# Kernel tuning notes

Measured on AMD Instinct MI355X. Metric: run time of the kernel, lower is better.

## Reference

```python
import jax, jax.numpy as jnp
import numpy as np

B, S, D, H = 4, 2048, 512, 8
DK = D // H


def setup_inputs() -> dict:
    key = jax.random.key(0)
    ks = jax.random.split(key, 8)
    std = 1.0 / np.sqrt(D)
    return {
        "query": jax.random.normal(ks[0], (B, S, D), jnp.float32),
        "key": jax.random.normal(ks[1], (B, S, D), jnp.float32),
        "value": jax.random.normal(ks[2], (B, S, D), jnp.float32),
        "Wq": jax.random.normal(ks[3], (D, D), jnp.float32) * std,
        "Wk": jax.random.normal(ks[4], (D, D), jnp.float32) * std,
        "Wv": jax.random.normal(ks[5], (D, D), jnp.float32) * std,
        "Wo": jax.random.normal(ks[6], (D, D), jnp.float32) * std,
        "bo": jnp.zeros((D,), jnp.float32),
    }


def reference(query, key, value, Wq, Wk, Wv, Wo, bo):
    # nn.Linear stores weight [out, in]; y = x @ W.T
    def split_heads(x):  # [B,S,D] -> [B,H,S,DK]
        return x.reshape(B, S, H, DK).transpose(0, 2, 1, 3)

    Q = split_heads(query @ Wq.T)
    K = split_heads(key @ Wk.T)
    V = split_heads(value @ Wv.T)
    scale = jnp.sqrt(jnp.asarray(DK, Q.dtype))
    scores = jnp.einsum("bhqd,bhkd->bhqk", Q, K) / scale  # [B,H,S,S]
    attn = jax.nn.softmax(scores, axis=-1)  # dropout=0 / eval mode
    ctx = jnp.einsum("bhqk,bhkd->bhqd", attn, V)
    ctx = ctx.transpose(0, 2, 1, 3).reshape(B, S, D)
    return ctx @ Wo.T + bo
```

## Files before the change

### kernel.cpp

```cpp
#include <hip/hip_runtime.h>
#include <hip/hip_bf16.h>
#include <stdint.h>

#define DEV __device__ __forceinline__

typedef __attribute__((ext_vector_type(8))) __bf16 bf16x8;
typedef __attribute__((ext_vector_type(4))) float f32x4;
typedef __attribute__((ext_vector_type(16))) float f32x16;
typedef __attribute__((ext_vector_type(4))) short short4v;
typedef __attribute__((ext_vector_type(8))) short short8v;
typedef __attribute__((ext_vector_type(4))) unsigned int uint4v;
typedef __attribute__((ext_vector_type(2))) unsigned int uint2v;

constexpr int B_ = 4, S_ = 2048, D_ = 512, H_ = 8, DK_ = 64;
constexpr int M_ = B_ * S_;
constexpr int K_ = D_;

DEV unsigned short f2bf(float f) {
  unsigned int u = __builtin_bit_cast(unsigned int, f);
  unsigned int r = (u + 0x7fffu + ((u >> 16) & 1u)) >> 16;
  return (unsigned short)r;
}

DEV void gld16(const void* g, void* l) {
  __builtin_amdgcn_global_load_lds(
      (const __attribute__((address_space(1))) unsigned int*)g,
      (__attribute__((address_space(3))) unsigned int*)l, 16, 0, 0);
}

DEV f32x4 mfma16(bf16x8 a, bf16x8 b, f32x4 c) {
  return __builtin_amdgcn_mfma_f32_16x16x32_bf16(a, b, c, 0, 0, 0);
}
DEV f32x16 mfma32(bf16x8 a, bf16x8 b, f32x16 c) {
  return __builtin_amdgcn_mfma_f32_32x32x16_bf16(a, b, c, 0, 0, 0);
}

DEV short4v tr16(const void* p) {
  short4v d;
  asm volatile("ds_read_b64_tr_b16 %0, %1"
               : "=v"(d)
               : "v"((const __attribute__((address_space(3))) char*)p));
  return d;
}

DEV unsigned pkbf(float a, float b) {
  unsigned r;
  asm("v_cvt_pk_bf16_f32 %0, %1, %2" : "=v"(r) : "v"(a), "v"(b));
  return r;
}

DEV void pl32swap(unsigned& a, unsigned& b) {
  asm volatile("v_permlane32_swap_b32 %0, %1" : "+v"(a), "+v"(b));
}

__global__ __launch_bounds__(256) void convert_w(
    const float* __restrict__ w0, const float* __restrict__ w1,
    const float* __restrict__ w2, const float* __restrict__ w3,
    unsigned short* __restrict__ o0, unsigned short* __restrict__ o1,
    unsigned short* __restrict__ o2, unsigned short* __restrict__ o3)
{
  int u = blockIdx.x * 256 + threadIdx.x;
  int t = u >> 16, off = (u & 65535) * 4;
  const float* src = (t == 0) ? w0 : (t == 1) ? w1 : (t == 2) ? w2 : w3;
  unsigned short* dst = (t == 0) ? o0 : (t == 1) ? o1 : (t == 2) ? o2 : o3;
  float4 f = *(const float4*)(src + off);
  short4v o;
  o.x = (short)f2bf(f.x); o.y = (short)f2bf(f.y);
  o.z = (short)f2bf(f.z); o.w = (short)f2bf(f.w);
  *(short4v*)(dst + off) = o;
}

__global__ __launch_bounds__(256, 3) void gemm_qkv(
    const float* __restrict__ A0, const float* __restrict__ A1,
    const float* __restrict__ A2,
    const unsigned short* __restrict__ W0, const unsigned short* __restrict__ W1,
    const unsigned short* __restrict__ W2,
    unsigned short* __restrict__ O0, unsigned short* __restrict__ O1,
    unsigned short* __restrict__ O2)
{
  constexpr int BM = 128, BN = 128, BK = 64, NKT = K_ / BK;
  __shared__ unsigned short As[BM * BK];
  __shared__ unsigned short Bs[BN * BK];
  const int tid = threadIdx.x, lane = tid & 63, wave = tid >> 6;
  const int z = blockIdx.z;
  const float* A = (z == 0) ? A0 : (z == 1 ? A1 : A2);
  const unsigned short* W = (z == 0) ? W0 : (z == 1 ? W1 : W2);
  unsigned short* outH = (z == 0) ? O0 : (z == 1 ? O1 : O2);
  const int bn0 = blockIdx.x * BN, bm0 = blockIdx.y * BM;
  const int wr = (wave >> 1) * 64, wc = (wave & 1) * 64;
  const int frow = lane & 15, fk16 = (lane >> 4) * 16;

  const int srow = tid >> 1, scol = (tid & 1) * 32;
  const float* asrc = A + (size_t)(bm0 + srow) * K_ + scol;
  const int abase = srow * 128 + scol * 2, asw = (srow & 7) << 4;

  const char* srcB[4];
  int dstB[4];
#pragma unroll
  for (int i = 0; i < 4; ++i) {
    int o = (wave * 4 + i) * 1024;
    int ol = o + lane * 16;
    int row = ol >> 7, off = (ol ^ ((row & 7) << 4)) & 127;
    srcB[i] = (const char*)W + (size_t)(bn0 + row) * (K_ * 2) + off;
    dstB[i] = o;
  }

  f32x4 acc[4][4];
#pragma unroll
  for (int i = 0; i < 4; ++i)
#pragma unroll
    for (int j = 0; j < 4; ++j)
#pragma unroll
      for (int r = 0; r < 4; ++r) acc[i][j][r] = 0.f;

  float4 xv[8];
#pragma unroll
  for (int j = 0; j < 8; ++j) xv[j] = *(const float4*)(asrc + j * 4);

  for (int kt = 0; kt < NKT; ++kt) {
    __syncthreads();
    {
      unsigned dw[16];
#pragma unroll
      for (int j = 0; j < 8; ++j) {
        dw[2 * j]     = pkbf(xv[j].x, xv[j].y);
        dw[2 * j + 1] = pkbf(xv[j].z, xv[j].w);
      }
#pragma unroll
      for (int c = 0; c < 4; ++c) {
        uint4v q = {dw[4 * c], dw[4 * c + 1], dw[4 * c + 2], dw[4 * c + 3]};
        *(uint4v*)((char*)As + ((abase + c * 16) ^ asw)) = q;
      }
    }
#pragma unroll
    for (int i = 0; i < 4; ++i) gld16(srcB[i] + kt * 128, (char*)Bs + dstB[i]);
    __syncthreads();
    if (kt + 1 < NKT) {
#pragma unroll
      for (int j = 0; j < 8; ++j)
        xv[j] = *(const float4*)(asrc + (kt + 1) * 64 + j * 4);
    }
#pragma unroll
    for (int kc = 0; kc < 2; ++kc) {
      bf16x8 a[4], b[4];
#pragma unroll
      for (int i = 0; i < 4; ++i) {
        int row = wr + i * 16 + frow;
        a[i] = *(const bf16x8*)((const char*)As +
                ((row * 128 + kc * 64 + fk16) ^ ((row & 7) << 4)));
      }
#pragma unroll
      for (int j = 0; j < 4; ++j) {
        int row = wc + j * 16 + frow;
        b[j] = *(const bf16x8*)((const char*)Bs +
                ((row * 128 + kc * 64 + fk16) ^ ((row & 7) << 4)));
      }
      __builtin_amdgcn_s_setprio(1);
#pragma unroll
      for (int i = 0; i < 4; ++i)
#pragma unroll
        for (int j = 0; j < 4; ++j)
          acc[i][j] = mfma16(a[i], b[j], acc[i][j]);
      __builtin_amdgcn_s_setprio(0);
    }
  }

  const int r0 = (lane >> 4) * 4, cn = lane & 15;
#pragma unroll
  for (int i = 0; i < 4; ++i)
#pragma unroll
    for (int j = 0; j < 4; ++j)
#pragma unroll
      for (int r = 0; r < 4; ++r) {
        int gm = bm0 + wr + i * 16 + r0 + r;
        int gn = bn0 + wc + j * 16 + cn;
        outH[(size_t)gm * D_ + gn] = f2bf(acc[i][j][r]);
      }
}

__global__ __launch_bounds__(256, 4) void gemm_out(
    const unsigned short* __restrict__ A, const unsigned short* __restrict__ W,
    float* __restrict__ outF, const float* __restrict__ bias)
{
  constexpr int BM = 64, BN = 128, BK = 64, NKT = K_ / BK, AFR = 2;
  __shared__ unsigned short As[BM * BK];
  __shared__ unsigned short Bs[BN * BK];
  const int tid = threadIdx.x, lane = tid & 63, wave = tid >> 6;
  const int bn0 = blockIdx.x * BN, bm0 = blockIdx.y * BM;
  const int wr = (wave >> 1) * 32, wc = (wave & 1) * 64;
  const int frow = lane & 15, fk16 = (lane >> 4) * 16;

  const char* srcA[AFR];
  int dstA[AFR];
#pragma unroll
  for (int i = 0; i < AFR; ++i) {
    int o = (wave * AFR + i) * 1024;
    int ol = o + lane * 16;
    int row = ol >> 7, off = (ol ^ ((row & 7) << 4)) & 127;
    srcA[i] = (const char*)A + (size_t)(bm0 + row) * (K_ * 2) + off;
    dstA[i] = o;
  }
  const char* srcB[4];
  int dstB[4];
#pragma unroll
  for (int i = 0; i < 4; ++i) {
    int o = (wave * 4 + i) * 1024;
    int ol = o + lane * 16;
    int row = ol >> 7, off = (ol ^ ((row & 7) << 4)) & 127;
    srcB[i] = (const char*)W + (size_t)(bn0 + row) * (K_ * 2) + off;
    dstB[i] = o;
  }

  f32x4 acc[AFR][4];
#pragma unroll
  for (int i = 0; i < AFR; ++i)
#pragma unroll
    for (int j = 0; j < 4; ++j)
#pragma unroll
      for (int r = 0; r < 4; ++r) acc[i][j][r] = 0.f;

  for (int kt = 0; kt < NKT; ++kt) {
    __syncthreads();
#pragma unroll
    for (int i = 0; i < AFR; ++i) gld16(srcA[i] + kt * 128, (char*)As + dstA[i]);
#pragma unroll
    for (int i = 0; i < 4; ++i)   gld16(srcB[i] + kt * 128, (char*)Bs + dstB[i]);
    __syncthreads();
#pragma unroll
    for (int kc = 0; kc < 2; ++kc) {
      bf16x8 a[AFR], b[4];
#pragma unroll
      for (int i = 0; i < AFR; ++i) {
        int row = wr + i * 16 + frow;
        a[i] = *(const bf16x8*)((const char*)As +
                ((row * 128 + kc * 64 + fk16) ^ ((row & 7) << 4)));
      }
#pragma unroll
      for (int j = 0; j < 4; ++j) {
        int row = wc + j * 16 + frow;
        b[j] = *(const bf16x8*)((const char*)Bs +
                ((row * 128 + kc * 64 + fk16) ^ ((row & 7) << 4)));
      }
      __builtin_amdgcn_s_setprio(1);
#pragma unroll
      for (int i = 0; i < AFR; ++i)
#pragma unroll
        for (int j = 0; j < 4; ++j)
          acc[i][j] = mfma16(a[i], b[j], acc[i][j]);
      __builtin_amdgcn_s_setprio(0);
    }
  }

  const int r0 = (lane >> 4) * 4, cn = lane & 15;
  float bv[4];
#pragma unroll
  for (int j = 0; j < 4; ++j) bv[j] = bias[bn0 + wc + j * 16 + cn];
#pragma unroll
  for (int i = 0; i < AFR; ++i)
#pragma unroll
    for (int j = 0; j < 4; ++j)
#pragma unroll
      for (int r = 0; r < 4; ++r) {
        int gm = bm0 + wr + i * 16 + r0 + r;
        int gn = bn0 + wc + j * 16 + cn;
        outF[(size_t)gm * D_ + gn] = acc[i][j][r] + bv[j];
      }
}

__global__ __launch_bounds__(256, 2) void attn(
    const unsigned short* __restrict__ Qm, const unsigned short* __restrict__ Km,
    const unsigned short* __restrict__ Vm, unsigned short* __restrict__ Ctx)
{
  constexpr int QB = 128, KVB = 64, NT = S_ / KVB;
  __shared__ unsigned short Qs[QB * DK_];
  __shared__ unsigned short Kd[2][KVB * DK_];
  __shared__ unsigned short Vd[2][KVB * DK_];
  const int tid = threadIdx.x, lane = tid & 63, wave = tid >> 6;
  const int hi = lane >> 5, l31 = lane & 31, g1 = (lane >> 4) & 1;
  const int bh = blockIdx.y, q0 = blockIdx.x * QB;
  const int bq = bh >> 3, hh = bh & 7;
  const char* Qg = (const char*)(Qm + ((size_t)bq * S_ + q0) * D_ + hh * DK_);
  const char* Kg = (const char*)(Km + (size_t)bq * S_ * D_ + hh * DK_);
  const char* Vg = (const char*)(Vm + (size_t)bq * S_ * D_ + hh * DK_);

  auto stageSwz = [&](const char* gbase, unsigned short* lds, int o) {
    int ol = o + lane * 16;
    int row = ol >> 7, off = (ol ^ ((row & 7) << 4)) & 127;
    gld16(gbase + (size_t)row * 1024 + off, (char*)lds + o);
  };
  auto stageVt = [&](const char* gbase, unsigned short* lds, int o) {
    int ol = o + lane * 16;
    int E0 = ol >> 1;
    int st = E0 >> 6, rr = (E0 >> 4) & 3, c0 = E0 & 15;
    int kk = (st >> 2) * 4 + rr, dd = (st & 3) * 16 + c0;
    gld16(gbase + (size_t)kk * 1024 + dd * 2, (char*)lds + o);
  };

#pragma unroll
  for (int i = 0; i < 4; ++i) stageSwz(Qg, Qs, (wave * 4 + i) * 1024);
#pragma unroll
  for (int i = 0; i < 2; ++i) stageSwz(Kg, Kd[0], (wave * 2 + i) * 1024);
#pragma unroll
  for (int i = 0; i < 2; ++i) stageVt(Vg, Vd[0], (wave * 2 + i) * 1024);
  __syncthreads();

  bf16x8 qf[4];
  {
    int row = wave * 32 + l31;
    int rb = row * 128, sw = (row & 7) << 4;
#pragma unroll
    for (int c = 0; c < 4; ++c)
      qf[c] = *(const bf16x8*)((const char*)Qs + ((rb + c * 32 + hi * 16) ^ sw));
  }

  f32x16 oacc[2];
#pragma unroll
  for (int dt = 0; dt < 2; ++dt)
#pragma unroll
    for (int r = 0; r < 16; ++r) oacc[dt][r] = 0.f;
  float m2 = -1e30f, lsum = 0.f;
  constexpr float SCL2 = 0.125f * 1.44269504089f;

  short4v va[4][2][2];
  bf16x8 pfrag[4];
#pragma unroll
  for (int c = 0; c < 4; ++c) {
#pragma unroll
    for (int dt = 0; dt < 2; ++dt) {
      va[c][dt][0] = short4v{0, 0, 0, 0};
      va[c][dt][1] = short4v{0, 0, 0, 0};
    }
    uint4v zz = {0u, 0u, 0u, 0u};
    pfrag[c] = __builtin_bit_cast(bf16x8, zz);
  }

  int cur = 0;
  for (int t = 0; t < NT; ++t) {
    if (t + 1 < NT) {
      const char* Kg1 = Kg + (size_t)(t + 1) * KVB * 1024;
      const char* Vg1 = Vg + (size_t)(t + 1) * KVB * 1024;
#pragma unroll
      for (int i = 0; i < 2; ++i) stageSwz(Kg1, Kd[cur ^ 1], (wave * 2 + i) * 1024);
#pragma unroll
      for (int i = 0; i < 2; ++i) stageVt(Vg1, Vd[cur ^ 1], (wave * 2 + i) * 1024);
    }

    f32x16 sacc[2];
#pragma unroll
    for (int k2 = 0; k2 < 2; ++k2)
#pragma unroll
      for (int r = 0; r < 16; ++r) sacc[k2][r] = 0.f;
    __builtin_amdgcn_s_setprio(1);
#pragma unroll
    for (int c = 0; c < 4; ++c) {
#pragma unroll
      for (int k2 = 0; k2 < 2; ++k2) {
        int row = k2 * 32 + l31;
        bf16x8 kf = *(const bf16x8*)((const char*)Kd[cur] +
                     ((row * 128 + c * 32 + hi * 16) ^ ((row & 7) << 4)));
        sacc[k2] = mfma32(kf, qf[c], sacc[k2]);
      }
    }
#pragma unroll
    for (int c = 0; c < 4; ++c)
#pragma unroll
      for (int dt = 0; dt < 2; ++dt) {
        short8v vv = __builtin_shufflevector(va[c][dt][0], va[c][dt][1],
                                             0, 1, 2, 3, 4, 5, 6, 7);
        oacc[dt] = mfma32(__builtin_bit_cast(bf16x8, vv), pfrag[c], oacc[dt]);
      }
    __builtin_amdgcn_s_setprio(0);

    float mloc = sacc[0][0];
#pragma unroll
    for (int k2 = 0; k2 < 2; ++k2)
#pragma unroll
      for (int r = 0; r < 16; ++r) mloc = fmaxf(mloc, sacc[k2][r]);
    mloc = fmaxf(mloc, __shfl_xor(mloc, 32));
    float m2n = fmaxf(m2, mloc * SCL2);
    float alpha = __builtin_amdgcn_exp2f(m2 - m2n);
    m2 = m2n;
    float psum = 0.f;
#pragma unroll
    for (int k2 = 0; k2 < 2; ++k2)
#pragma unroll
      for (int r = 0; r < 16; ++r) {
        float p = __builtin_amdgcn_exp2f(fmaf(sacc[k2][r], SCL2, -m2n));
        sacc[k2][r] = p;
        psum += p;
      }
    psum += __shfl_xor(psum, 32);
    lsum = lsum * alpha + psum;

#pragma unroll
    for (int dt = 0; dt < 2; ++dt)
#pragma unroll
      for (int r = 0; r < 16; ++r) oacc[dt][r] *= alpha;

#pragma unroll
    for (int c = 0; c < 4; ++c)
#pragma unroll
      for (int dt = 0; dt < 2; ++dt) {
        int st = 16 * c + 8 * hi + 2 * dt + g1;
        const char* ad = (const char*)Vd[cur] + st * 128 + (lane & 15) * 8;
        va[c][dt][0] = tr16(ad);
        va[c][dt][1] = tr16(ad + 512);
      }
#pragma unroll
    for (int c = 0; c < 4; ++c) {
      const f32x16& P = sacc[c >> 1];
      const int b = (c & 1) * 8;
      unsigned d0 = pkbf(P[b + 0], P[b + 1]);
      unsigned d1 = pkbf(P[b + 2], P[b + 3]);
      unsigned d2 = pkbf(P[b + 4], P[b + 5]);
      unsigned d3 = pkbf(P[b + 6], P[b + 7]);
      pl32swap(d0, d2);
      pl32swap(d1, d3);
      uint4v pi = {d0, d1, d2, d3};
      pfrag[c] = __builtin_bit_cast(bf16x8, pi);
    }

    __syncthreads();
    cur ^= 1;
  }

  __builtin_amdgcn_s_setprio(1);
#pragma unroll
  for (int c = 0; c < 4; ++c)
#pragma unroll
    for (int dt = 0; dt < 2; ++dt) {
      short8v vv = __builtin_shufflevector(va[c][dt][0], va[c][dt][1],
                                           0, 1, 2, 3, 4, 5, 6, 7);
      oacc[dt] = mfma32(__builtin_bit_cast(bf16x8, vv), pfrag[c], oacc[dt]);
    }
  __builtin_amdgcn_s_setprio(0);

  const float inv = 1.f / lsum;
  unsigned short* crow =
      Ctx + ((size_t)bq * S_ + q0 + wave * 32 + l31) * D_ + hh * DK_;
#pragma unroll
  for (int dt = 0; dt < 2; ++dt)
#pragma unroll
    for (int g = 0; g < 4; ++g) {
      uint2v pk;
      pk.x = pkbf(oacc[dt][4 * g + 0] * inv, oacc[dt][4 * g + 1] * inv);
      pk.y = pkbf(oacc[dt][4 * g + 2] * inv, oacc[dt][4 * g + 3] * inv);
      *(uint2v*)(crow + dt * 32 + 8 * g + 4 * hi) = pk;
    }
}

extern "C" void kernel_launch(void* const* d_in, const int* in_sizes, int n_in,
                              void* d_out, int out_size, void* d_ws, size_t ws_size,
                              hipStream_t stream) {
  const float* q  = (const float*)d_in[0];
  const float* k  = (const float*)d_in[1];
  const float* v  = (const float*)d_in[2];
  const float* wq = (const float*)d_in[3];
  const float* wk = (const float*)d_in[4];
  const float* wv = (const float*)d_in[5];
  const float* wo = (const float*)d_in[6];
  const float* bo = (const float*)d_in[7];
  float* out = (float*)d_out;

  constexpr size_t NX = (size_t)M_ * D_;
  constexpr size_t NW = (size_t)D_ * D_;
  char* ws = (char*)d_ws;
  unsigned short* Wqb = (unsigned short*)ws; ws += NW * 2;
  unsigned short* Wkb = (unsigned short*)ws; ws += NW * 2;
  unsigned short* Wvb = (unsigned short*)ws; ws += NW * 2;
  unsigned short* Wob = (unsigned short*)ws; ws += NW * 2;
  unsigned short* Qbf = (unsigned short*)ws; ws += NX * 2;
  unsigned short* Kbf = (unsigned short*)ws; ws += NX * 2;
  unsigned short* Vbf = (unsigned short*)ws; ws += NX * 2;
  unsigned short* Cx  = (unsigned short*)ws; ws += NX * 2;

  convert_w<<<1024, 256, 0, stream>>>(wq, wk, wv, wo, Wqb, Wkb, Wvb, Wob);
  gemm_qkv<<<dim3(4, 64, 3), 256, 0, stream>>>(
      q, k, v, Wqb, Wkb, Wvb, Qbf, Kbf, Vbf);
  attn<<<dim3(S_ / 128, B_ * H_), 256, 0, stream>>>(Qbf, Kbf, Vbf, Cx);
  gemm_out<<<dim3(4, 128), 256, 0, stream>>>(Cx, Wob, out, bo);
}
```

Before: 201.0 us.

## Add lazy softmax rescaling and precompute LDS addresses in attention loop

Precomputes the global source and LDS destination addresses for K/V staging outside the loop, uses immediate offsets for transposed LDS reads, and unrolls the loop by two so the double-buffer indices are compile-time constants. It also adds a lazy online-softmax rescale: the running max and the accumulator rescale are updated only when some lane's new max exceeds the old one by more than 8 in log2 units. The row-sum uses four partial sums and the max uses a tree reduction to shorten dependency chains. The cost is extra code size, plus exponentials that can reach up to 2^8 before a rescale.

```diff
diff --git a/kernel.cpp b/kernel.cpp
--- a/kernel.cpp
+++ b/kernel.cpp
@@ -35,11 +35,12 @@
   return __builtin_amdgcn_mfma_f32_32x32x16_bf16(a, b, c, 0, 0, 0);
 }
 
-DEV short4v tr16(const void* p) {
+template <int OFF>
+DEV short4v tr16o(const void* p) {
   short4v d;
-  asm volatile("ds_read_b64_tr_b16 %0, %1"
+  asm volatile("ds_read_b64_tr_b16 %0, %1 offset:%2"
                : "=v"(d)
-               : "v"((const __attribute__((address_space(3))) char*)p));
+               : "v"((const __attribute__((address_space(3))) char*)p), "i"(OFF));
   return d;
 }
 
@@ -283,25 +284,38 @@
   const char* Kg = (const char*)(Km + (size_t)bq * S_ * D_ + hh * DK_);
   const char* Vg = (const char*)(Vm + (size_t)bq * S_ * D_ + hh * DK_);
 
-  auto stageSwz = [&](const char* gbase, unsigned short* lds, int o) {
+  const char* srcK[2];
+  const char* srcV[2];
+  int dstKV[2];
+#pragma unroll
+  for (int i = 0; i < 2; ++i) {
+    int o = (wave * 2 + i) * 1024;
+    int ol = o + lane * 16;
+    {
+      int row = ol >> 7, off = (ol ^ ((row & 7) << 4)) & 127;
+      srcK[i] = Kg + (size_t)row * 1024 + off;
+    }
+    {
+      int E0 = ol >> 1;
+      int st = E0 >> 6, rr = (E0 >> 4) & 3, c0 = E0 & 15;
+      int kk = (st >> 2) * 4 + rr, dd = (st & 3) * 16 + c0;
+      srcV[i] = Vg + (size_t)kk * 1024 + dd * 2;
+    }
+    dstKV[i] = o;
+  }
+
+#pragma unroll
+  for (int i = 0; i < 4; ++i) {
+    int o = (wave * 4 + i) * 1024;
     int ol = o + lane * 16;
     int row = ol >> 7, off = (ol ^ ((row & 7) << 4)) & 127;
-    gld16(gbase + (size_t)row * 1024 + off, (char*)lds + o);
-  };
-  auto stageVt = [&](const char* gbase, unsigned short* lds, int o) {
-    int ol = o + lane * 16;
-    int E0 = ol >> 1;
-    int st = E0 >> 6, rr = (E0 >> 4) & 3, c0 = E0 & 15;
-    int kk = (st >> 2) * 4 + rr, dd = (st & 3) * 16 + c0;
-    gld16(gbase + (size_t)kk * 1024 + dd * 2, (char*)lds + o);
-  };
-
-#pragma unroll
-  for (int i = 0; i < 4; ++i) stageSwz(Qg, Qs, (wave * 4 + i) * 1024);
-#pragma unroll
-  for (int i = 0; i < 2; ++i) stageSwz(Kg, Kd[0], (wave * 2 + i) * 1024);
-#pragma unroll
-  for (int i = 0; i < 2; ++i) stageVt(Vg, Vd[0], (wave * 2 + i) * 1024);
+    gld16(Qg + (size_t)row * 1024 + off, (char*)Qs + o);
+  }
+#pragma unroll
+  for (int i = 0; i < 2; ++i) {
+    gld16(srcK[i], (char*)Kd[0] + dstKV[i]);
+    gld16(srcV[i], (char*)Vd[0] + dstKV[i]);
+  }
   __syncthreads();
 
   bf16x8 qf[4];
@@ -313,6 +327,13 @@
       qf[c] = *(const bf16x8*)((const char*)Qs + ((rb + c * 32 + hi * 16) ^ sw));
   }
 
+  int bofs[4];
+  {
+    const int swk = (l31 & 7) << 4;
+#pragma unroll
+    for (int c = 0; c < 4; ++c) bofs[c] = (c * 32 + hi * 16) ^ swk;
+  }
+
   f32x16 oacc[2];
 #pragma unroll
   for (int dt = 0; dt < 2; ++dt)
@@ -334,15 +355,15 @@
     pfrag[c] = __builtin_bit_cast(bf16x8, zz);
   }
 
-  int cur = 0;
-  for (int t = 0; t < NT; ++t) {
-    if (t + 1 < NT) {
-      const char* Kg1 = Kg + (size_t)(t + 1) * KVB * 1024;
-      const char* Vg1 = Vg + (size_t)(t + 1) * KVB * 1024;
-#pragma unroll
-      for (int i = 0; i < 2; ++i) stageSwz(Kg1, Kd[cur ^ 1], (wave * 2 + i) * 1024);
-#pragma unroll
-      for (int i = 0; i < 2; ++i) stageVt(Vg1, Vd[cur ^ 1], (wave * 2 + i) * 1024);
+  auto tile = [&](const unsigned short* Kbuf, const unsigned short* Vbuf,
+                  unsigned short* KbufN, unsigned short* VbufN,
+                  int tnext, bool doStage) {
+    if (doStage) {
+#pragma unroll
+      for (int i = 0; i < 2; ++i) {
+        gld16(srcK[i] + (size_t)tnext * 65536, (char*)KbufN + dstKV[i]);
+        gld16(srcV[i] + (size_t)tnext * 65536, (char*)VbufN + dstKV[i]);
+      }
     }
 
     f32x16 sacc[2];
@@ -350,16 +371,14 @@
     for (int k2 = 0; k2 < 2; ++k2)
 #pragma unroll
       for (int r = 0; r < 16; ++r) sacc[k2][r] = 0.f;
+    const char* kb = (const char*)Kbuf + l31 * 128;
     __builtin_amdgcn_s_setprio(1);
 #pragma unroll
     for (int c = 0; c < 4; ++c) {
-#pragma unroll
-      for (int k2 = 0; k2 < 2; ++k2) {
-        int row = k2 * 32 + l31;
-        bf16x8 kf = *(const bf16x8*)((const char*)Kd[cur] +
-                     ((row * 128 + c * 32 + hi * 16) ^ ((row & 7) << 4)));
-        sacc[k2] = mfma32(kf, qf[c], sacc[k2]);
-      }
+      bf16x8 kf0 = *(const bf16x8*)(kb + bofs[c]);
+      bf16x8 kf1 = *(const bf16x8*)(kb + bofs[c] + 4096);
+      sacc[0] = mfma32(kf0, qf[c], sacc[0]);
+      sacc[1] = mfma32(kf1, qf[c], sacc[1]);
     }
 #pragma unroll
     for (int c = 0; c < 4; ++c)
@@ -371,41 +390,45 @@
       }
     __builtin_amdgcn_s_setprio(0);
 
-    float mloc = sacc[0][0];
+    float mx[16];
+#pragma unroll
+    for (int r = 0; r < 16; ++r) mx[r] = fmaxf(sacc[0][r], sacc[1][r]);
+#pragma unroll
+    for (int st = 8; st >= 1; st >>= 1)
+#pragma unroll
+      for (int r = 0; r < st; ++r) mx[r] = fmaxf(mx[r], mx[r + st]);
+    float mloc = fmaxf(mx[0], __shfl_xor(mx[0], 32)) * SCL2;
+    if (!__all(mloc <= m2 + 8.f)) {
+      float m2n = fmaxf(m2, mloc);
+      float alpha = __builtin_amdgcn_exp2f(m2 - m2n);
+      m2 = m2n;
+      lsum *= alpha;
+#pragma unroll
+      for (int dt = 0; dt < 2; ++dt)
+#pragma unroll
+        for (int r = 0; r < 16; ++r) oacc[dt][r] *= alpha;
+    }
+    float ps[4] = {0.f, 0.f, 0.f, 0.f};
 #pragma unroll
     for (int k2 = 0; k2 < 2; ++k2)
 #pragma unroll
-      for (int r = 0; r < 16; ++r) mloc = fmaxf(mloc, sacc[k2][r]);
-    mloc = fmaxf(mloc, __shfl_xor(mloc, 32));
-    float m2n = fmaxf(m2, mloc * SCL2);
-    float alpha = __builtin_amdgcn_exp2f(m2 - m2n);
-    m2 = m2n;
-    float psum = 0.f;
-#pragma unroll
-    for (int k2 = 0; k2 < 2; ++k2)
-#pragma unroll
       for (int r = 0; r < 16; ++r) {
-        float p = __builtin_amdgcn_exp2f(fmaf(sacc[k2][r], SCL2, -m2n));
+        float p = __builtin_amdgcn_exp2f(fmaf(sacc[k2][r], SCL2, -m2));
         sacc[k2][r] = p;
-        psum += p;
-      }
+        ps[r & 3] += p;
+      }
+    float psum = (ps[0] + ps[1]) + (ps[2] + ps[3]);
     psum += __shfl_xor(psum, 32);
-    lsum = lsum * alpha + psum;
-
-#pragma unroll
-    for (int dt = 0; dt < 2; ++dt)
-#pragma unroll
-      for (int r = 0; r < 16; ++r) oacc[dt][r] *= alpha;
-
-#pragma unroll
-    for (int c = 0; c < 4; ++c)
-#pragma unroll
-      for (int dt = 0; dt < 2; ++dt) {
-        int st = 16 * c + 8 * hi + 2 * dt + g1;
-        const char* ad = (const char*)Vd[cur] + st * 128 + (lane & 15) * 8;
-        va[c][dt][0] = tr16(ad);
-        va[c][dt][1] = tr16(ad + 512);
-      }
+    lsum += psum;
+
+    const char* vt = (const char*)Vbuf + hi * 1024 + g1 * 128 + (lane & 15) * 8;
+#define TR16(c, dt)                                                    \
+    va[c][dt][0] = tr16o<(c) * 2048 + (dt) * 256>(vt);                 \
+    va[c][dt][1] = tr16o<(c) * 2048 + (dt) * 256 + 512>(vt);
+    TR16(0, 0) TR16(0, 1) TR16(1, 0) TR16(1, 1)
+    TR16(2, 0) TR16(2, 1) TR16(3, 0) TR16(3, 1)
+#undef TR16
+
 #pragma unroll
     for (int c = 0; c < 4; ++c) {
       const f32x16& P = sacc[c >> 1];
@@ -421,7 +444,11 @@
     }
 
     __syncthreads();
-    cur ^= 1;
+  };
+
+  for (int tb = 0; tb < NT; tb += 2) {
+    tile(Kd[0], Vd[0], Kd[1], Vd[1], tb + 1, true);
+    tile(Kd[1], Vd[1], Kd[0], Vd[0], tb + 2, tb + 2 < NT);
   }
 
   __builtin_amdgcn_s_setprio(1);
```

After: 199.3 us. No clear change (-0.8%).
